# Optimization experiments

Measured on AMD Instinct MI355X. Metric: run time of the kernel, lower is better.

## Reference

```python
import jax, jax.numpy as jnp
import numpy as np

V_MIN = -10.0
V_MAX = 10.0
NUM_ATOMS = 251
B = 131072
N_OBS = 128
N_ACT = 32
HID = 512


def _ln(x, g, b, eps=1e-5):
    m = jnp.mean(x, axis=-1, keepdims=True)
    v = jnp.var(x, axis=-1, keepdims=True)
    return (x - m) * jax.lax.rsqrt(v + eps) * g + b


def setup_inputs() -> dict:
    key = jax.random.key(0)
    ks = jax.random.split(key, 16)

    def lin(k, fi, fo):
        kw, kb = jax.random.split(k)
        lim = 1.0 / np.sqrt(fi)
        W = jax.random.uniform(kw, (fi, fo), jnp.float32, -lim, lim)
        b = jax.random.uniform(kb, (fo,), jnp.float32, -lim, lim)
        return W, b

    W1, b1 = lin(ks[0], N_OBS + N_ACT, HID)
    W2, b2 = lin(ks[1], HID, HID // 2)
    W3, b3 = lin(ks[2], HID // 2, HID // 4)
    W4, b4 = lin(ks[3], HID // 4, NUM_ATOMS)

    return {
        "obs": jax.random.normal(ks[4], (B, N_OBS), jnp.float32),
        "actions": jax.random.normal(ks[5], (B, N_ACT), jnp.float32),
        "rewards": jax.random.normal(ks[6], (B,), jnp.float32),
        "bootstrap": (jax.random.uniform(ks[7], (B,)) > 0.05).astype(jnp.float32),
        "discount": jnp.full((B,), 0.99, jnp.float32),
        "q_support": jnp.linspace(V_MIN, V_MAX, NUM_ATOMS, dtype=jnp.float32),
        "W1": W1, "b1": b1, "g1": jnp.ones((HID,), jnp.float32), "be1": jnp.zeros((HID,), jnp.float32),
        "W2": W2, "b2": b2, "g2": jnp.ones((HID // 2,), jnp.float32), "be2": jnp.zeros((HID // 2,), jnp.float32),
        "W3": W3, "b3": b3, "g3": jnp.ones((HID // 4,), jnp.float32), "be3": jnp.zeros((HID // 4,), jnp.float32),
        "W4": W4, "b4": b4,
    }


def _net(obs, actions, W1, b1, g1, be1, W2, b2, g2, be2, W3, b3, g3, be3, W4, b4):
    x = jnp.concatenate([obs, actions], axis=1)
    x = jax.nn.silu(_ln(x @ W1 + b1, g1, be1))
    x = jax.nn.silu(_ln(x @ W2 + b2, g2, be2))
    x = jax.nn.silu(_ln(x @ W3 + b3, g3, be3))
    return x @ W4 + b4  # [B, NUM_ATOMS] logits


def reference(obs, actions, rewards, bootstrap, discount, q_support,
              W1, b1, g1, be1, W2, b2, g2, be2, W3, b3, g3, be3, W4, b4):
    # C51 categorical projection (DistributionalQNetwork.projection)
    delta_z = (V_MAX - V_MIN) / (NUM_ATOMS - 1)
    bsz = rewards.shape[0]
    target_z = rewards[:, None] + bootstrap[:, None] * discount[:, None] * q_support[None, :]
    target_z = jnp.clip(target_z, V_MIN, V_MAX)
    b = (target_z - V_MIN) / delta_z  # fractional bin positions [B, A]
    lower = jnp.floor(b).astype(jnp.int32)
    upper = jnp.ceil(b).astype(jnp.int32)
    is_integer = upper == lower
    lower_mask = (lower > 0) & is_integer
    upper_mask = (lower == 0) & is_integer
    lower = jnp.where(lower_mask, lower - 1, lower)
    upper = jnp.where(upper_mask, upper + 1, upper)

    logits = _net(obs, actions, W1, b1, g1, be1, W2, b2, g2, be2, W3, b3, g3, be3, W4, b4)
    next_dist = jax.nn.softmax(logits, axis=1)

    offset = (jnp.arange(bsz, dtype=jnp.int32) * NUM_ATOMS)[:, None]  # [B,1]
    max_index = bsz * NUM_ATOMS - 1
    li = jnp.clip((lower + offset).reshape(-1), 0, max_index)
    ui = jnp.clip((upper + offset).reshape(-1), 0, max_index)

    w_lo = (next_dist * (upper.astype(jnp.float32) - b)).reshape(-1)
    w_hi = (next_dist * (b - lower.astype(jnp.float32))).reshape(-1)

    proj = jnp.zeros((bsz * NUM_ATOMS,), next_dist.dtype)
    proj = proj.at[li].add(w_lo).at[ui].add(w_hi)
    return proj.reshape(bsz, NUM_ATOMS)
```

## Files before the change

### kernel.cpp

```cpp
#include <hip/hip_runtime.h>


#define THREADS 256

typedef __attribute__((ext_vector_type(8))) short short8v;
typedef __attribute__((ext_vector_type(4))) float f32x4;

__device__ __forceinline__ unsigned short f2bf(float f) {
  union { float f; unsigned u; } v; v.f = f;
  unsigned u = v.u;
  u += 0x7fffu + ((u >> 16) & 1u);
  return (unsigned short)(u >> 16);
}
__device__ __forceinline__ unsigned pack2bf(float a, float b) {
  return (unsigned)f2bf(a) | ((unsigned)f2bf(b) << 16);
}

__global__ void prep_kernel(const float* __restrict__ W1, const float* __restrict__ W2,
                            const float* __restrict__ W3, const float* __restrict__ W4,
                            unsigned short* __restrict__ ws) {
  int i = blockIdx.x * THREADS + threadIdx.x;
  if (i < 81920) {
    int n = i / 160, k = i - n * 160;
    ws[i] = f2bf(W1[k * 512 + n]);
  } else if (i < 212992) {
    int j = i - 81920; int n = j >> 9, k = j & 511;
    ws[i] = f2bf(W2[k * 256 + n]);
  } else if (i < 245760) {
    int j = i - 212992; int n = j >> 8, k = j & 255;
    ws[i] = f2bf(W3[k * 128 + n]);
  } else if (i < 278528) {
    int j = i - 245760; int n = j >> 7, k = j & 127;
    ws[i] = (n < 251) ? f2bf(W4[k * 251 + n]) : (unsigned short)0;
  }
}

#define OFF_H1  0
#define OFF_H2  32768
#define OFF_X   49152
#define OFF_ZS  59392
#define OFF_B4  60416
#define OFF_RED 61440
#define LDS_TOTAL 62464

template<int KD, int NFT>
__device__ __forceinline__ void gemm_w(const unsigned short* __restrict__ WT,
                                       const unsigned char* __restrict__ Hb,
                                       int fbase, f32x4 (&acc)[NFT][2]) {
  const int lane = threadIdx.x & 63;
  const int lm = lane & 15, kg = lane >> 4;
#pragma unroll 4
  for (int ks = 0; ks < KD / 32; ++ks) {
    const int kk = ks * 32 + kg * 8;
    short8v b[2];
#pragma unroll
    for (int rt = 0; rt < 2; ++rt) {
      const int r = rt * 16 + lm;
      int byte = r * (KD * 2) + kk * 2;
      byte ^= ((r & 7) << 4);
      b[rt] = *(const short8v*)(Hb + byte);
    }
#pragma unroll
    for (int ft = 0; ft < NFT; ++ft) {
      const short8v a = *(const short8v*)(WT + (size_t)(fbase + ft * 16 + lm) * KD + kk);
      acc[ft][0] = __builtin_amdgcn_mfma_f32_16x16x32_bf16(a, b[0], acc[ft][0], 0, 0, 0);
      acc[ft][1] = __builtin_amdgcn_mfma_f32_16x16x32_bf16(a, b[1], acc[ft][1], 0, 0, 0);
    }
  }
}

template<int ND, int NFT>
__device__ __forceinline__ void ln_silu_store(
    f32x4 (&acc)[NFT][2],
    const float* __restrict__ bias, const float* __restrict__ g,
    const float* __restrict__ be, unsigned char* __restrict__ Hb,
    float* __restrict__ redL, int fq)
{
  const int lane = threadIdx.x & 63;
  const int lm = lane & 15, kg = lane >> 4;
  const int fq0 = fq * (ND / 4);
  float s[2] = {0.f, 0.f}, q[2] = {0.f, 0.f};
#pragma unroll
  for (int ft = 0; ft < NFT; ++ft) {
    const int f0 = fq0 + ft * 16 + kg * 4;
    const f32x4 bb = *(const f32x4*)(bias + f0);
#pragma unroll
    for (int rt = 0; rt < 2; ++rt)
#pragma unroll
      for (int rg = 0; rg < 4; ++rg) {
        float x = acc[ft][rt][rg] + bb[rg];
        acc[ft][rt][rg] = x;
        s[rt] += x; q[rt] += x * x;
      }
  }
#pragma unroll
  for (int rt = 0; rt < 2; ++rt) {
    s[rt] += __shfl_xor(s[rt], 16); s[rt] += __shfl_xor(s[rt], 32);
    q[rt] += __shfl_xor(q[rt], 16); q[rt] += __shfl_xor(q[rt], 32);
  }
  if (lane < 16) {
#pragma unroll
    for (int rt = 0; rt < 2; ++rt) {
      redL[((rt * 16 + lm) * 4 + fq) * 2    ] = s[rt];
      redL[((rt * 16 + lm) * 4 + fq) * 2 + 1] = q[rt];
    }
  }
  __syncthreads();
  float mean[2], rstd[2];
#pragma unroll
  for (int rt = 0; rt < 2; ++rt) {
    const int row = rt * 16 + lm;
    float S = redL[row * 8 + 0] + redL[row * 8 + 2] + redL[row * 8 + 4] + redL[row * 8 + 6];
    float Q = redL[row * 8 + 1] + redL[row * 8 + 3] + redL[row * 8 + 5] + redL[row * 8 + 7];
    float m = S * (1.0f / ND);
    float v = Q * (1.0f / ND) - m * m;
    mean[rt] = m; rstd[rt] = rsqrtf(v + 1e-5f);
  }
#pragma unroll
  for (int ft = 0; ft < NFT; ++ft) {
    const int f0 = fq0 + ft * 16 + kg * 4;
    const f32x4 g4 = *(const f32x4*)(g + f0);
    const f32x4 e4 = *(const f32x4*)(be + f0);
#pragma unroll
    for (int rt = 0; rt < 2; ++rt) {
      const int row = rt * 16 + lm;
      float h[4];
#pragma unroll
      for (int rg = 0; rg < 4; ++rg) {
        float y = (acc[ft][rt][rg] - mean[rt]) * rstd[rt] * g4[rg] + e4[rg];
        h[rg] = y * (1.0f / (1.0f + __expf(-y)));
      }
      uint2 w; w.x = pack2bf(h[0], h[1]); w.y = pack2bf(h[2], h[3]);
      int byte = row * (ND * 2) + f0 * 2;
      byte ^= ((row & 7) << 4);
      *(uint2*)(Hb + byte) = w;
    }
  }
}

__global__ __launch_bounds__(THREADS, 2) void fused_kernel(
    const float* __restrict__ obs, const float* __restrict__ actions,
    const float* __restrict__ rewards, const float* __restrict__ bootstrap,
    const float* __restrict__ discount, const float* __restrict__ q_support,
    const float* __restrict__ b1, const float* __restrict__ g1, const float* __restrict__ be1,
    const float* __restrict__ b2, const float* __restrict__ g2, const float* __restrict__ be2,
    const float* __restrict__ b3, const float* __restrict__ g3, const float* __restrict__ be3,
    const float* __restrict__ b4,
    const unsigned short* __restrict__ ws,
    float* __restrict__ out)
{
  __shared__ __align__(16) unsigned char smem[LDS_TOTAL];
  const int tid  = threadIdx.x;
  const int fq   = tid >> 6;
  const int lane = tid & 63;
  const int lm   = lane & 15;
  const int kg   = lane >> 4;
  const int row0 = blockIdx.x * 32;

  const unsigned short* W1T = ws;
  const unsigned short* W2T = ws + 81920;
  const unsigned short* W3T = ws + 212992;
  const unsigned short* W4T = ws + 245760;

  float* zsL  = (float*)(smem + OFF_ZS);
  float* b4L  = (float*)(smem + OFF_B4);
  float* redL = (float*)(smem + OFF_RED);

  float rw[2], bt[2], dc[2];
#pragma unroll
  for (int rt = 0; rt < 2; ++rt) {
    const int r = row0 + rt * 16 + lm;
    rw[rt] = rewards[r]; bt[rt] = bootstrap[r]; dc[rt] = discount[r];
  }

  zsL[tid] = (tid < 251) ? q_support[tid] : 0.f;
  b4L[tid] = (tid < 251) ? b4[tid] : 0.f;

  {
    unsigned char* Xb = smem + OFF_X;
#pragma unroll
    for (int it = 0; it < 5; ++it) {
      const int qq = it * THREADS + tid;
      const int r  = qq / 40;
      const int c4 = (qq - r * 40) * 4;
      float4 v;
      if (c4 < 128) v = *(const float4*)(obs + (size_t)(row0 + r) * 128 + c4);
      else          v = *(const float4*)(actions + (size_t)(row0 + r) * 32 + (c4 - 128));
      uint2 w; w.x = pack2bf(v.x, v.y); w.y = pack2bf(v.z, v.w);
      int byte = r * 320 + c4 * 2;
      byte ^= ((r & 7) << 4);
      *(uint2*)(Xb + byte) = w;
    }
  }
  __syncthreads();

  f32x4 acc1[8][2];
#pragma unroll
  for (int i = 0; i < 8; ++i) { acc1[i][0] = f32x4{0,0,0,0}; acc1[i][1] = f32x4{0,0,0,0}; }
  gemm_w<160, 8>(W1T, smem + OFF_X, fq * 128, acc1);
  ln_silu_store<512, 8>(acc1, b1, g1, be1, smem + OFF_H1, redL, fq);
  __syncthreads();

  f32x4 acc2[4][2];
#pragma unroll
  for (int i = 0; i < 4; ++i) { acc2[i][0] = f32x4{0,0,0,0}; acc2[i][1] = f32x4{0,0,0,0}; }
  gemm_w<512, 4>(W2T, smem + OFF_H1, fq * 64, acc2);
  ln_silu_store<256, 4>(acc2, b2, g2, be2, smem + OFF_H2, redL, fq);
  float* projL = (float*)(smem + OFF_H1);
  for (int i = tid; i < 32 * 251; i += THREADS) projL[i] = 0.f;
  __syncthreads();

  f32x4 acc3[2][2];
#pragma unroll
  for (int i = 0; i < 2; ++i) { acc3[i][0] = f32x4{0,0,0,0}; acc3[i][1] = f32x4{0,0,0,0}; }
  gemm_w<256, 2>(W3T, smem + OFF_H2, fq * 32, acc3);
  ln_silu_store<128, 2>(acc3, b3, g3, be3, smem + OFF_X, redL, fq);
  __syncthreads();

  f32x4 acc4[4][2];
#pragma unroll
  for (int i = 0; i < 4; ++i) { acc4[i][0] = f32x4{0,0,0,0}; acc4[i][1] = f32x4{0,0,0,0}; }
  gemm_w<128, 4>(W4T, smem + OFF_X, fq * 64, acc4);

  float lv[4][2][4];
#pragma unroll
  for (int ft = 0; ft < 4; ++ft) {
    const int f0 = fq * 64 + ft * 16 + kg * 4;
    const f32x4 bb = *(const f32x4*)(b4L + f0);
#pragma unroll
    for (int rt = 0; rt < 2; ++rt)
#pragma unroll
      for (int rg = 0; rg < 4; ++rg) {
        const int f = f0 + rg;
        lv[ft][rt][rg] = (f < 251) ? (acc4[ft][rt][rg] + bb[rg]) : -1e30f;
      }
  }

#pragma unroll
  for (int rt = 0; rt < 2; ++rt) {
    float m = lv[0][rt][0];
#pragma unroll
    for (int ft = 0; ft < 4; ++ft)
#pragma unroll
      for (int rg = 0; rg < 4; ++rg) m = fmaxf(m, lv[ft][rt][rg]);
    m = fmaxf(m, __shfl_xor(m, 16));
    m = fmaxf(m, __shfl_xor(m, 32));
    if (lane < 16) redL[(rt * 16 + lm) * 4 + fq] = m;
  }
  __syncthreads();
  float gm[2];
#pragma unroll
  for (int rt = 0; rt < 2; ++rt) {
    const int row = rt * 16 + lm;
    gm[rt] = fmaxf(fmaxf(redL[row * 4 + 0], redL[row * 4 + 1]),
                   fmaxf(redL[row * 4 + 2], redL[row * 4 + 3]));
  }
  __syncthreads();
#pragma unroll
  for (int rt = 0; rt < 2; ++rt) {
    float E = 0.f;
#pragma unroll
    for (int ft = 0; ft < 4; ++ft)
#pragma unroll
      for (int rg = 0; rg < 4; ++rg) {
        float e = __expf(lv[ft][rt][rg] - gm[rt]);
        lv[ft][rt][rg] = e;
        E += e;
      }
    E += __shfl_xor(E, 16); E += __shfl_xor(E, 32);
    if (lane < 16) redL[(rt * 16 + lm) * 4 + fq] = E;
  }
  __syncthreads();
  float inv[2];
#pragma unroll
  for (int rt = 0; rt < 2; ++rt) {
    const int row = rt * 16 + lm;
    inv[rt] = 1.0f / (redL[row * 4 + 0] + redL[row * 4 + 1] +
                      redL[row * 4 + 2] + redL[row * 4 + 3]);
  }

  constexpr float DZF = 20.0f / 250.0f;
#pragma unroll
  for (int ft = 0; ft < 4; ++ft) {
    const int f0 = fq * 64 + ft * 16 + kg * 4;
    const f32x4 z4 = *(const f32x4*)(zsL + f0);
#pragma unroll
    for (int rt = 0; rt < 2; ++rt) {
      const int base = (rt * 16 + lm) * 251;
      const float bd = __fmul_rn(bt[rt], dc[rt]);
#pragma unroll
      for (int rg = 0; rg < 4; ++rg) {
        const int f = f0 + rg;
        if (f < 251) {
          const float p = lv[ft][rt][rg] * inv[rt];
          float t = __fadd_rn(rw[rt], __fmul_rn(bd, z4[rg]));
          t = fminf(fmaxf(t, -10.0f), 10.0f);
          const float bfr = __fdiv_rn(__fsub_rn(t, -10.0f), DZF);
          const float fl = floorf(bfr), fu = ceilf(bfr);
          int l = (int)fl, u = (int)fu;
          if (fl == fu) { if (l > 0) --l; else ++u; }
          atomicAdd(projL + base + l, p * ((float)u - bfr));
          atomicAdd(projL + base + u, p * (bfr - (float)l));
        }
      }
    }
  }
  __syncthreads();

  const float4* ps = (const float4*)projL;
  float4* po = (float4*)(out + (size_t)row0 * 251);
  for (int i = tid; i < 2008; i += THREADS) po[i] = ps[i];
}

extern "C" void kernel_launch(void* const* d_in, const int* in_sizes, int n_in,
                              void* d_out, int out_size, void* d_ws, size_t ws_size,
                              hipStream_t stream) {
  const float* obs  = (const float*)d_in[0];
  const float* act  = (const float*)d_in[1];
  const float* rew  = (const float*)d_in[2];
  const float* boot = (const float*)d_in[3];
  const float* disc = (const float*)d_in[4];
  const float* zs   = (const float*)d_in[5];
  const float* W1   = (const float*)d_in[6];
  const float* b1   = (const float*)d_in[7];
  const float* g1   = (const float*)d_in[8];
  const float* be1  = (const float*)d_in[9];
  const float* W2   = (const float*)d_in[10];
  const float* b2   = (const float*)d_in[11];
  const float* g2   = (const float*)d_in[12];
  const float* be2  = (const float*)d_in[13];
  const float* W3   = (const float*)d_in[14];
  const float* b3   = (const float*)d_in[15];
  const float* g3   = (const float*)d_in[16];
  const float* be3  = (const float*)d_in[17];
  const float* W4   = (const float*)d_in[18];
  const float* b4   = (const float*)d_in[19];
  unsigned short* wsp = (unsigned short*)d_ws;

  const int Bn = in_sizes[2];
  prep_kernel<<<(278528 + THREADS - 1) / THREADS, THREADS, 0, stream>>>(W1, W2, W3, W4, wsp);
  fused_kernel<<<Bn / 32, THREADS, 0, stream>>>(obs, act, rew, boot, disc, zs,
      b1, g1, be1, b2, g2, be2, b3, g3, be3, b4, wsp, (float*)d_out);
}
```

Before: 533.9 us.

## Split each 32-row tile across 8 waves and shrink LDS footprint

Doubles the block to 512 threads (8 waves), so each wave covers half as many output features per layer. Accumulator register use per wave drops and occupancy rises (launch bounds 6). LDS is reduced by ping-ponging two activation buffers and zeroing the projection buffer after layer 4, which also allows more resident blocks. The cost is more cross-wave LayerNorm and softmax reduction work and more barriers, and each weight fragment is reused across fewer features per wave.

```diff
diff --git a/kernel.cpp b/kernel.cpp
--- a/kernel.cpp
+++ b/kernel.cpp
@@ -1,7 +1,8 @@
 #include <hip/hip_runtime.h>
 
 
-#define THREADS 256
+#define THREADS 512
+#define PREP_THREADS 256
 
 typedef __attribute__((ext_vector_type(8))) short short8v;
 typedef __attribute__((ext_vector_type(4))) float f32x4;
@@ -19,7 +20,7 @@
 __global__ void prep_kernel(const float* __restrict__ W1, const float* __restrict__ W2,
                             const float* __restrict__ W3, const float* __restrict__ W4,
                             unsigned short* __restrict__ ws) {
-  int i = blockIdx.x * THREADS + threadIdx.x;
+  int i = blockIdx.x * PREP_THREADS + threadIdx.x;
   if (i < 81920) {
     int n = i / 160, k = i - n * 160;
     ws[i] = f2bf(W1[k * 512 + n]);
@@ -35,13 +36,12 @@
   }
 }
 
-#define OFF_H1  0
-#define OFF_H2  32768
-#define OFF_X   49152
-#define OFF_ZS  59392
-#define OFF_B4  60416
-#define OFF_RED 61440
-#define LDS_TOTAL 62464
+#define OFF_A   0
+#define OFF_B   32768
+#define OFF_ZS  49152
+#define OFF_B4  50176
+#define OFF_RED 51200
+#define LDS_TOTAL 53376
 
 template<int KD, int NFT>
 __device__ __forceinline__ void gemm_w(const unsigned short* __restrict__ WT,
@@ -74,15 +74,14 @@
     f32x4 (&acc)[NFT][2],
     const float* __restrict__ bias, const float* __restrict__ g,
     const float* __restrict__ be, unsigned char* __restrict__ Hb,
-    float* __restrict__ redL, int fq)
+    float* __restrict__ redL, int fbase, int fq)
 {
   const int lane = threadIdx.x & 63;
   const int lm = lane & 15, kg = lane >> 4;
-  const int fq0 = fq * (ND / 4);
   float s[2] = {0.f, 0.f}, q[2] = {0.f, 0.f};
 #pragma unroll
   for (int ft = 0; ft < NFT; ++ft) {
-    const int f0 = fq0 + ft * 16 + kg * 4;
+    const int f0 = fbase + ft * 16 + kg * 4;
     const f32x4 bb = *(const f32x4*)(bias + f0);
 #pragma unroll
     for (int rt = 0; rt < 2; ++rt)
@@ -101,8 +100,8 @@
   if (lane < 16) {
 #pragma unroll
     for (int rt = 0; rt < 2; ++rt) {
-      redL[((rt * 16 + lm) * 4 + fq) * 2    ] = s[rt];
-      redL[((rt * 16 + lm) * 4 + fq) * 2 + 1] = q[rt];
+      redL[(rt * 16 + lm) * 17 + fq * 2    ] = s[rt];
+      redL[(rt * 16 + lm) * 17 + fq * 2 + 1] = q[rt];
     }
   }
   __syncthreads();
@@ -110,15 +109,19 @@
 #pragma unroll
   for (int rt = 0; rt < 2; ++rt) {
     const int row = rt * 16 + lm;
-    float S = redL[row * 8 + 0] + redL[row * 8 + 2] + redL[row * 8 + 4] + redL[row * 8 + 6];
-    float Q = redL[row * 8 + 1] + redL[row * 8 + 3] + redL[row * 8 + 5] + redL[row * 8 + 7];
+    float S = 0.f, Q = 0.f;
+#pragma unroll
+    for (int w = 0; w < 8; ++w) {
+      S += redL[row * 17 + w * 2];
+      Q += redL[row * 17 + w * 2 + 1];
+    }
     float m = S * (1.0f / ND);
     float v = Q * (1.0f / ND) - m * m;
     mean[rt] = m; rstd[rt] = rsqrtf(v + 1e-5f);
   }
 #pragma unroll
   for (int ft = 0; ft < NFT; ++ft) {
-    const int f0 = fq0 + ft * 16 + kg * 4;
+    const int f0 = fbase + ft * 16 + kg * 4;
     const f32x4 g4 = *(const f32x4*)(g + f0);
     const f32x4 e4 = *(const f32x4*)(be + f0);
 #pragma unroll
@@ -138,7 +141,7 @@
   }
 }
 
-__global__ __launch_bounds__(THREADS, 2) void fused_kernel(
+__global__ __launch_bounds__(THREADS, 6) void fused_kernel(
     const float* __restrict__ obs, const float* __restrict__ actions,
     const float* __restrict__ rewards, const float* __restrict__ bootstrap,
     const float* __restrict__ discount, const float* __restrict__ q_support,
@@ -173,14 +176,14 @@
     rw[rt] = rewards[r]; bt[rt] = bootstrap[r]; dc[rt] = discount[r];
   }
 
-  zsL[tid] = (tid < 251) ? q_support[tid] : 0.f;
-  b4L[tid] = (tid < 251) ? b4[tid] : 0.f;
+  if (tid < 256) {
+    zsL[tid] = (tid < 251) ? q_support[tid] : 0.f;
+    b4L[tid] = (tid < 251) ? b4[tid] : 0.f;
+  }
 
   {
-    unsigned char* Xb = smem + OFF_X;
-#pragma unroll
-    for (int it = 0; it < 5; ++it) {
-      const int qq = it * THREADS + tid;
+    unsigned char* Xb = smem + OFF_B;
+    for (int qq = tid; qq < 1280; qq += THREADS) {
       const int r  = qq / 40;
       const int c4 = (qq - r * 40) * 4;
       float4 v;
@@ -194,38 +197,35 @@
   }
   __syncthreads();
 
-  f32x4 acc1[8][2];
-#pragma unroll
-  for (int i = 0; i < 8; ++i) { acc1[i][0] = f32x4{0,0,0,0}; acc1[i][1] = f32x4{0,0,0,0}; }
-  gemm_w<160, 8>(W1T, smem + OFF_X, fq * 128, acc1);
-  ln_silu_store<512, 8>(acc1, b1, g1, be1, smem + OFF_H1, redL, fq);
-  __syncthreads();
-
-  f32x4 acc2[4][2];
-#pragma unroll
-  for (int i = 0; i < 4; ++i) { acc2[i][0] = f32x4{0,0,0,0}; acc2[i][1] = f32x4{0,0,0,0}; }
-  gemm_w<512, 4>(W2T, smem + OFF_H1, fq * 64, acc2);
-  ln_silu_store<256, 4>(acc2, b2, g2, be2, smem + OFF_H2, redL, fq);
-  float* projL = (float*)(smem + OFF_H1);
-  for (int i = tid; i < 32 * 251; i += THREADS) projL[i] = 0.f;
-  __syncthreads();
-
-  f32x4 acc3[2][2];
-#pragma unroll
-  for (int i = 0; i < 2; ++i) { acc3[i][0] = f32x4{0,0,0,0}; acc3[i][1] = f32x4{0,0,0,0}; }
-  gemm_w<256, 2>(W3T, smem + OFF_H2, fq * 32, acc3);
-  ln_silu_store<128, 2>(acc3, b3, g3, be3, smem + OFF_X, redL, fq);
-  __syncthreads();
-
-  f32x4 acc4[4][2];
-#pragma unroll
-  for (int i = 0; i < 4; ++i) { acc4[i][0] = f32x4{0,0,0,0}; acc4[i][1] = f32x4{0,0,0,0}; }
-  gemm_w<128, 4>(W4T, smem + OFF_X, fq * 64, acc4);
-
-  float lv[4][2][4];
-#pragma unroll
-  for (int ft = 0; ft < 4; ++ft) {
-    const int f0 = fq * 64 + ft * 16 + kg * 4;
+  f32x4 acc1[4][2];
+#pragma unroll
+  for (int i = 0; i < 4; ++i) { acc1[i][0] = f32x4{0,0,0,0}; acc1[i][1] = f32x4{0,0,0,0}; }
+  gemm_w<160, 4>(W1T, smem + OFF_B, fq * 64, acc1);
+  ln_silu_store<512, 4>(acc1, b1, g1, be1, smem + OFF_A, redL, fq * 64, fq);
+  __syncthreads();
+
+  f32x4 acc2[2][2];
+#pragma unroll
+  for (int i = 0; i < 2; ++i) { acc2[i][0] = f32x4{0,0,0,0}; acc2[i][1] = f32x4{0,0,0,0}; }
+  gemm_w<512, 2>(W2T, smem + OFF_A, fq * 32, acc2);
+  ln_silu_store<256, 2>(acc2, b2, g2, be2, smem + OFF_B, redL, fq * 32, fq);
+  __syncthreads();
+
+  f32x4 acc3[1][2];
+  acc3[0][0] = f32x4{0,0,0,0}; acc3[0][1] = f32x4{0,0,0,0};
+  gemm_w<256, 1>(W3T, smem + OFF_B, fq * 16, acc3);
+  ln_silu_store<128, 1>(acc3, b3, g3, be3, smem + OFF_A, redL, fq * 16, fq);
+  __syncthreads();
+
+  f32x4 acc4[2][2];
+#pragma unroll
+  for (int i = 0; i < 2; ++i) { acc4[i][0] = f32x4{0,0,0,0}; acc4[i][1] = f32x4{0,0,0,0}; }
+  gemm_w<128, 2>(W4T, smem + OFF_A, fq * 32, acc4);
+
+  float lv[2][2][4];
+#pragma unroll
+  for (int ft = 0; ft < 2; ++ft) {
+    const int f0 = fq * 32 + ft * 16 + kg * 4;
     const f32x4 bb = *(const f32x4*)(b4L + f0);
 #pragma unroll
     for (int rt = 0; rt < 2; ++rt)
@@ -240,27 +240,33 @@
   for (int rt = 0; rt < 2; ++rt) {
     float m = lv[0][rt][0];
 #pragma unroll
-    for (int ft = 0; ft < 4; ++ft)
+    for (int ft = 0; ft < 2; ++ft)
 #pragma unroll
       for (int rg = 0; rg < 4; ++rg) m = fmaxf(m, lv[ft][rt][rg]);
     m = fmaxf(m, __shfl_xor(m, 16));
     m = fmaxf(m, __shfl_xor(m, 32));
-    if (lane < 16) redL[(rt * 16 + lm) * 4 + fq] = m;
-  }
-  __syncthreads();
+    if (lane < 16) redL[(rt * 16 + lm) * 9 + fq] = m;
+  }
+  __syncthreads();
+
+  float* projL = (float*)(smem + OFF_A);
+  for (int i = tid; i < 32 * 251; i += THREADS) projL[i] = 0.f;
+
   float gm[2];
 #pragma unroll
   for (int rt = 0; rt < 2; ++rt) {
     const int row = rt * 16 + lm;
-    gm[rt] = fmaxf(fmaxf(redL[row * 4 + 0], redL[row * 4 + 1]),
-                   fmaxf(redL[row * 4 + 2], redL[row * 4 + 3]));
+    float m = redL[row * 9];
+#pragma unroll
+    for (int w = 1; w < 8; ++w) m = fmaxf(m, redL[row * 9 + w]);
+    gm[rt] = m;
   }
   __syncthreads();
 #pragma unroll
   for (int rt = 0; rt < 2; ++rt) {
     float E = 0.f;
 #pragma unroll
-    for (int ft = 0; ft < 4; ++ft)
+    for (int ft = 0; ft < 2; ++ft)
 #pragma unroll
       for (int rg = 0; rg < 4; ++rg) {
         float e = __expf(lv[ft][rt][rg] - gm[rt]);
@@ -268,21 +274,23 @@
         E += e;
       }
     E += __shfl_xor(E, 16); E += __shfl_xor(E, 32);
-    if (lane < 16) redL[(rt * 16 + lm) * 4 + fq] = E;
+    if (lane < 16) redL[(rt * 16 + lm) * 9 + fq] = E;
   }
   __syncthreads();
   float inv[2];
 #pragma unroll
   for (int rt = 0; rt < 2; ++rt) {
     const int row = rt * 16 + lm;
-    inv[rt] = 1.0f / (redL[row * 4 + 0] + redL[row * 4 + 1] +
-                      redL[row * 4 + 2] + redL[row * 4 + 3]);
+    float E = 0.f;
+#pragma unroll
+    for (int w = 0; w < 8; ++w) E += redL[row * 9 + w];
+    inv[rt] = 1.0f / E;
   }
 
   constexpr float DZF = 20.0f / 250.0f;
 #pragma unroll
-  for (int ft = 0; ft < 4; ++ft) {
-    const int f0 = fq * 64 + ft * 16 + kg * 4;
+  for (int ft = 0; ft < 2; ++ft) {
+    const int f0 = fq * 32 + ft * 16 + kg * 4;
     const f32x4 z4 = *(const f32x4*)(zsL + f0);
 #pragma unroll
     for (int rt = 0; rt < 2; ++rt) {
@@ -338,7 +346,8 @@
   unsigned short* wsp = (unsigned short*)d_ws;
 
   const int Bn = in_sizes[2];
-  prep_kernel<<<(278528 + THREADS - 1) / THREADS, THREADS, 0, stream>>>(W1, W2, W3, W4, wsp);
+  prep_kernel<<<(278528 + PREP_THREADS - 1) / PREP_THREADS, PREP_THREADS, 0, stream>>>(
+      W1, W2, W3, W4, wsp);
   fused_kernel<<<Bn / 32, THREADS, 0, stream>>>(obs, act, rew, boot, disc, zs,
       b1, g1, be1, b2, g2, be2, b3, g3, be3, b4, wsp, (float*)d_out);
 }
```

Result: slower. 574.3 us (+7.6%).

## Ping-pong LDS buffers to cut shared memory and raise occupancy

Applied to the files above, without the earlier changes.

Replaces the three separate activation buffers with two ping-pong LDS regions, shrinking shared memory per block from about 62KB to 52KB and raising launch bounds to 3 blocks per CU. The projection-buffer zeroing moves later, after the logits GEMM, because its region is now reused. The GEMM inner loop is fully unrolled with precomputed weight offsets and swizzled LDS pointers to reduce address arithmetic. Reduction scratch rows are padded (stride 9 and 5) to avoid bank conflicts. Allowing 3 blocks per CU puts a tighter limit on registers per thread, which may cause spills.

```diff
diff --git a/kernel.cpp b/kernel.cpp
--- a/kernel.cpp
+++ b/kernel.cpp
@@ -2,6 +2,7 @@
 
 
 #define THREADS 256
+#define PREP_THREADS 256
 
 typedef __attribute__((ext_vector_type(8))) short short8v;
 typedef __attribute__((ext_vector_type(4))) float f32x4;
@@ -19,7 +20,7 @@
 __global__ void prep_kernel(const float* __restrict__ W1, const float* __restrict__ W2,
                             const float* __restrict__ W3, const float* __restrict__ W4,
                             unsigned short* __restrict__ ws) {
-  int i = blockIdx.x * THREADS + threadIdx.x;
+  int i = blockIdx.x * PREP_THREADS + threadIdx.x;
   if (i < 81920) {
     int n = i / 160, k = i - n * 160;
     ws[i] = f2bf(W1[k * 512 + n]);
@@ -35,13 +36,12 @@
   }
 }
 
-#define OFF_H1  0
-#define OFF_H2  32768
-#define OFF_X   49152
-#define OFF_ZS  59392
-#define OFF_B4  60416
-#define OFF_RED 61440
-#define LDS_TOTAL 62464
+#define OFF_A   0
+#define OFF_B   32768
+#define OFF_ZS  49152
+#define OFF_B4  50176
+#define OFF_RED 51200
+#define LDS_TOTAL 52480
 
 template<int KD, int NFT>
 __device__ __forceinline__ void gemm_w(const unsigned short* __restrict__ WT,
@@ -49,22 +49,29 @@
                                        int fbase, f32x4 (&acc)[NFT][2]) {
   const int lane = threadIdx.x & 63;
   const int lm = lane & 15, kg = lane >> 4;
-#pragma unroll 4
+  int woff[NFT];
+#pragma unroll
+  for (int ft = 0; ft < NFT; ++ft)
+    woff[ft] = (fbase + ft * 16 + lm) * KD + kg * 8;
+  const unsigned char* bp[2][2];
+#pragma unroll
+  for (int rt = 0; rt < 2; ++rt) {
+    const int r = rt * 16 + lm;
+    const int swz = (r & 7) << 4;
+    const int base = r * (KD * 2) + kg * 16;
+    bp[rt][0] = Hb + ((base) ^ swz);
+    bp[rt][1] = Hb + ((base + 64) ^ swz);
+  }
+#pragma unroll
   for (int ks = 0; ks < KD / 32; ++ks) {
-    const int kk = ks * 32 + kg * 8;
-    short8v b[2];
-#pragma unroll
-    for (int rt = 0; rt < 2; ++rt) {
-      const int r = rt * 16 + lm;
-      int byte = r * (KD * 2) + kk * 2;
-      byte ^= ((r & 7) << 4);
-      b[rt] = *(const short8v*)(Hb + byte);
-    }
+    const int koff = (ks >> 1) * 128;
+    const short8v b0 = *(const short8v*)(bp[0][ks & 1] + koff);
+    const short8v b1 = *(const short8v*)(bp[1][ks & 1] + koff);
 #pragma unroll
     for (int ft = 0; ft < NFT; ++ft) {
-      const short8v a = *(const short8v*)(WT + (size_t)(fbase + ft * 16 + lm) * KD + kk);
-      acc[ft][0] = __builtin_amdgcn_mfma_f32_16x16x32_bf16(a, b[0], acc[ft][0], 0, 0, 0);
-      acc[ft][1] = __builtin_amdgcn_mfma_f32_16x16x32_bf16(a, b[1], acc[ft][1], 0, 0, 0);
+      const short8v a = *(const short8v*)(WT + woff[ft] + ks * 32);
+      acc[ft][0] = __builtin_amdgcn_mfma_f32_16x16x32_bf16(a, b0, acc[ft][0], 0, 0, 0);
+      acc[ft][1] = __builtin_amdgcn_mfma_f32_16x16x32_bf16(a, b1, acc[ft][1], 0, 0, 0);
     }
   }
 }
@@ -74,15 +81,14 @@
     f32x4 (&acc)[NFT][2],
     const float* __restrict__ bias, const float* __restrict__ g,
     const float* __restrict__ be, unsigned char* __restrict__ Hb,
-    float* __restrict__ redL, int fq)
+    float* __restrict__ redL, int fbase, int fq)
 {
   const int lane = threadIdx.x & 63;
   const int lm = lane & 15, kg = lane >> 4;
-  const int fq0 = fq * (ND / 4);
   float s[2] = {0.f, 0.f}, q[2] = {0.f, 0.f};
 #pragma unroll
   for (int ft = 0; ft < NFT; ++ft) {
-    const int f0 = fq0 + ft * 16 + kg * 4;
+    const int f0 = fbase + ft * 16 + kg * 4;
     const f32x4 bb = *(const f32x4*)(bias + f0);
 #pragma unroll
     for (int rt = 0; rt < 2; ++rt)
@@ -101,8 +107,8 @@
   if (lane < 16) {
 #pragma unroll
     for (int rt = 0; rt < 2; ++rt) {
-      redL[((rt * 16 + lm) * 4 + fq) * 2    ] = s[rt];
-      redL[((rt * 16 + lm) * 4 + fq) * 2 + 1] = q[rt];
+      redL[(rt * 16 + lm) * 9 + fq * 2    ] = s[rt];
+      redL[(rt * 16 + lm) * 9 + fq * 2 + 1] = q[rt];
     }
   }
   __syncthreads();
@@ -110,15 +116,19 @@
 #pragma unroll
   for (int rt = 0; rt < 2; ++rt) {
     const int row = rt * 16 + lm;
-    float S = redL[row * 8 + 0] + redL[row * 8 + 2] + redL[row * 8 + 4] + redL[row * 8 + 6];
-    float Q = redL[row * 8 + 1] + redL[row * 8 + 3] + redL[row * 8 + 5] + redL[row * 8 + 7];
+    float S = 0.f, Q = 0.f;
+#pragma unroll
+    for (int w = 0; w < 4; ++w) {
+      S += redL[row * 9 + w * 2];
+      Q += redL[row * 9 + w * 2 + 1];
+    }
     float m = S * (1.0f / ND);
     float v = Q * (1.0f / ND) - m * m;
     mean[rt] = m; rstd[rt] = rsqrtf(v + 1e-5f);
   }
 #pragma unroll
   for (int ft = 0; ft < NFT; ++ft) {
-    const int f0 = fq0 + ft * 16 + kg * 4;
+    const int f0 = fbase + ft * 16 + kg * 4;
     const f32x4 g4 = *(const f32x4*)(g + f0);
     const f32x4 e4 = *(const f32x4*)(be + f0);
 #pragma unroll
@@ -138,7 +148,7 @@
   }
 }
 
-__global__ __launch_bounds__(THREADS, 2) void fused_kernel(
+__global__ __launch_bounds__(THREADS, 3) void fused_kernel(
     const float* __restrict__ obs, const float* __restrict__ actions,
     const float* __restrict__ rewards, const float* __restrict__ bootstrap,
     const float* __restrict__ discount, const float* __restrict__ q_support,
@@ -177,7 +187,7 @@
   b4L[tid] = (tid < 251) ? b4[tid] : 0.f;
 
   {
-    unsigned char* Xb = smem + OFF_X;
+    unsigned char* Xb = smem + OFF_B;
 #pragma unroll
     for (int it = 0; it < 5; ++it) {
       const int qq = it * THREADS + tid;
@@ -197,30 +207,28 @@
   f32x4 acc1[8][2];
 #pragma unroll
   for (int i = 0; i < 8; ++i) { acc1[i][0] = f32x4{0,0,0,0}; acc1[i][1] = f32x4{0,0,0,0}; }
-  gemm_w<160, 8>(W1T, smem + OFF_X, fq * 128, acc1);
-  ln_silu_store<512, 8>(acc1, b1, g1, be1, smem + OFF_H1, redL, fq);
+  gemm_w<160, 8>(W1T, smem + OFF_B, fq * 128, acc1);
+  ln_silu_store<512, 8>(acc1, b1, g1, be1, smem + OFF_A, redL, fq * 128, fq);
   __syncthreads();
 
   f32x4 acc2[4][2];
 #pragma unroll
   for (int i = 0; i < 4; ++i) { acc2[i][0] = f32x4{0,0,0,0}; acc2[i][1] = f32x4{0,0,0,0}; }
-  gemm_w<512, 4>(W2T, smem + OFF_H1, fq * 64, acc2);
-  ln_silu_store<256, 4>(acc2, b2, g2, be2, smem + OFF_H2, redL, fq);
-  float* projL = (float*)(smem + OFF_H1);
-  for (int i = tid; i < 32 * 251; i += THREADS) projL[i] = 0.f;
+  gemm_w<512, 4>(W2T, smem + OFF_A, fq * 64, acc2);
+  ln_silu_store<256, 4>(acc2, b2, g2, be2, smem + OFF_B, redL, fq * 64, fq);
   __syncthreads();
 
   f32x4 acc3[2][2];
 #pragma unroll
   for (int i = 0; i < 2; ++i) { acc3[i][0] = f32x4{0,0,0,0}; acc3[i][1] = f32x4{0,0,0,0}; }
-  gemm_w<256, 2>(W3T, smem + OFF_H2, fq * 32, acc3);
-  ln_silu_store<128, 2>(acc3, b3, g3, be3, smem + OFF_X, redL, fq);
+  gemm_w<256, 2>(W3T, smem + OFF_B, fq * 32, acc3);
+  ln_silu_store<128, 2>(acc3, b3, g3, be3, smem + OFF_A, redL, fq * 32, fq);
   __syncthreads();
 
   f32x4 acc4[4][2];
 #pragma unroll
   for (int i = 0; i < 4; ++i) { acc4[i][0] = f32x4{0,0,0,0}; acc4[i][1] = f32x4{0,0,0,0}; }
-  gemm_w<128, 4>(W4T, smem + OFF_X, fq * 64, acc4);
+  gemm_w<128, 4>(W4T, smem + OFF_A, fq * 64, acc4);
 
   float lv[4][2][4];
 #pragma unroll
@@ -245,15 +253,21 @@
       for (int rg = 0; rg < 4; ++rg) m = fmaxf(m, lv[ft][rt][rg]);
     m = fmaxf(m, __shfl_xor(m, 16));
     m = fmaxf(m, __shfl_xor(m, 32));
-    if (lane < 16) redL[(rt * 16 + lm) * 4 + fq] = m;
-  }
-  __syncthreads();
+    if (lane < 16) redL[(rt * 16 + lm) * 5 + fq] = m;
+  }
+  __syncthreads();
+
+  float* projL = (float*)(smem + OFF_A);
+  for (int i = tid; i < 32 * 251; i += THREADS) projL[i] = 0.f;
+
   float gm[2];
 #pragma unroll
   for (int rt = 0; rt < 2; ++rt) {
     const int row = rt * 16 + lm;
-    gm[rt] = fmaxf(fmaxf(redL[row * 4 + 0], redL[row * 4 + 1]),
-                   fmaxf(redL[row * 4 + 2], redL[row * 4 + 3]));
+    float m = redL[row * 5];
+#pragma unroll
+    for (int w = 1; w < 4; ++w) m = fmaxf(m, redL[row * 5 + w]);
+    gm[rt] = m;
   }
   __syncthreads();
 #pragma unroll
@@ -268,15 +282,17 @@
         E += e;
       }
     E += __shfl_xor(E, 16); E += __shfl_xor(E, 32);
-    if (lane < 16) redL[(rt * 16 + lm) * 4 + fq] = E;
+    if (lane < 16) redL[(rt * 16 + lm) * 5 + fq] = E;
   }
   __syncthreads();
   float inv[2];
 #pragma unroll
   for (int rt = 0; rt < 2; ++rt) {
     const int row = rt * 16 + lm;
-    inv[rt] = 1.0f / (redL[row * 4 + 0] + redL[row * 4 + 1] +
-                      redL[row * 4 + 2] + redL[row * 4 + 3]);
+    float E = 0.f;
+#pragma unroll
+    for (int w = 0; w < 4; ++w) E += redL[row * 5 + w];
+    inv[rt] = 1.0f / E;
   }
 
   constexpr float DZF = 20.0f / 250.0f;
@@ -338,7 +354,8 @@
   unsigned short* wsp = (unsigned short*)d_ws;
 
   const int Bn = in_sizes[2];
-  prep_kernel<<<(278528 + THREADS - 1) / THREADS, THREADS, 0, stream>>>(W1, W2, W3, W4, wsp);
+  prep_kernel<<<(278528 + PREP_THREADS - 1) / PREP_THREADS, PREP_THREADS, 0, stream>>>(
+      W1, W2, W3, W4, wsp);
   fused_kernel<<<Bn / 32, THREADS, 0, stream>>>(obs, act, rew, boot, disc, zs,
       b1, g1, be1, b2, g2, be2, b3, g3, be3, b4, wsp, (float*)d_out);
 }
```

New measurement: 508.0 us. -4.9%, faster.
